# Performance work log

Hardware: AMD Instinct MI355X
Metric: run time of the kernel (lower is better)

## Reference

```python
import jax, jax.numpy as jnp
import numpy as np

LMAX = 3
NDEG = LMAX + 1            # degrees l = 0..3
MDIM = 2 * LMAX + 1        # padded m dimension (7)
K = 128                    # channels per degree
N = 4096                   # number of samples (atomic environments)
NITER = 2                  # number_of_iterations

# CG paths (l1, l2) -> L with |l1-l2| <= L <= min(l1+l2, LMAX); 34 paths
PATHS = [(l1, l2, L)
         for L in range(NDEG)
         for l1 in range(NDEG)
         for l2 in range(NDEG)
         if abs(l1 - l2) <= L <= l1 + l2]


def setup_inputs() -> dict:
    key = jax.random.key(0)
    k1, k2, k3, k4 = jax.random.split(key, 4)

    # zero-mask padded m components: valid m < 2l+1 per degree l
    mmask = (jnp.arange(MDIM)[None, :] < (2 * jnp.arange(NDEG) + 1)[:, None])
    mmask = mmask.astype(jnp.float32)                      # [NDEG, MDIM]

    feats = jax.random.normal(k1, (NDEG, N, MDIM, K), dtype=jnp.float32)
    feats = feats * mmask[:, None, :, None]

    # CG-like coefficients, zero-padded per path to [2l1+1, 2l2+1, 2L+1]
    umask = np.zeros((len(PATHS), MDIM, MDIM, MDIM), dtype=np.float32)
    for p, (l1, l2, L) in enumerate(PATHS):
        umask[p, :2 * l1 + 1, :2 * l2 + 1, :2 * L + 1] = 1.0
    U = jax.random.normal(k2, (len(PATHS), MDIM, MDIM, MDIM), dtype=jnp.float32)
    U = 0.1 * U * jnp.asarray(umask)

    scale = 1.0 / np.sqrt(K)
    mixer_W = scale * jax.random.normal(k3, (NITER + 1, NDEG, K, K), dtype=jnp.float32)
    iter_W = scale * jax.random.normal(k4, (NITER, NDEG, K, K), dtype=jnp.float32)

    return {"feats": feats, "U": U, "mixer_W": mixer_W, "iter_W": iter_W}


def spherical_linear(f, W):
    # per-degree channel mix: f [NDEG, N, MDIM, K], W [NDEG, K, K]
    return jnp.einsum('lnmk,lkj->lnmj', f, W)


def tensor_product(f1, f2, U):
    # channel-wise CG tensor product, summed over paths into each output degree L
    out = jnp.zeros_like(f1)
    for p, (l1, l2, L) in enumerate(PATHS):
        out = out.at[L].add(jnp.einsum('nak,nbk,abc->nck', f1[l1], f2[l2], U[p]))
    return out


def reference(feats, U, mixer_W, iter_W):
    # mixed_densities = [mixer(density) for mixer in self.mixers]
    mixed = [spherical_linear(feats, mixer_W[i]) for i in range(NITER + 1)]
    cur = mixed[0]
    # CG iterations: residual( linear( tensor_product(cur, mixed[t+1]) ) )
    for t in range(NITER):
        tp = tensor_product(cur, mixed[t + 1], U)
        cur = cur + spherical_linear(tp, iter_W[t])
    return cur
```

## Files before the change

kernel.cpp:

```cpp
#include <hip/hip_runtime.h>

#define NSAMP 4096
#define KCH   128
#define MDIM  7

typedef __attribute__((ext_vector_type(8))) short bf16x8;
typedef __attribute__((ext_vector_type(4))) float f32x4;
typedef __attribute__((ext_vector_type(4))) unsigned u32x4;

static constexpr int RB[4] = {0, 1, 4, 9};
static constexpr int RE[4] = {1, 4, 9, 16};
static constexpr int PR_L[16] = {0,1,1,1,2,2,2,2,2,3,3,3,3,3,3,3};
static constexpr int PR_M[16] = {0,0,1,2,0,1,2,3,4,0,1,2,3,4,5,6};

static constexpr int PIDX[4][4][4] = {
  { { 0,-1,-1,-1},{-1, 1,-1,-1},{-1,-1, 2,-1},{-1,-1,-1, 3} },
  { {-1, 4,-1,-1},{ 5, 6, 7,-1},{-1, 8, 9,10},{-1,-1,11,12} },
  { {-1,-1,13,-1},{-1,14,15,16},{17,18,19,20},{-1,21,22,23} },
  { {-1,-1,-1,24},{-1,-1,25,26},{-1,27,28,29},{30,31,32,33} }
};

static constexpr int ZL[12] = {0,0,0,0,0,0, 1,1,1,1, 2,2};
static constexpr int ZM[12] = {1,2,3,4,5,6, 3,4,5,6, 5,6};

#define WP_BYTES 1310720u
#define BG_BYTES 16384u

static __device__ __forceinline__ unsigned short f2bf(float x) {
    unsigned u = __builtin_bit_cast(unsigned, x);
    u = u + 0x7FFFu + ((u >> 16) & 1u);
    return (unsigned short)(u >> 16);
}
static __device__ __forceinline__ float bf2f(unsigned short h) {
    unsigned u = ((unsigned)h) << 16;
    return __builtin_bit_cast(float, u);
}

__global__ __launch_bounds__(256) void cg_prep(const float* __restrict__ mW,
                                               const float* __restrict__ iW,
                                               unsigned short* __restrict__ Wp)
{
    int gid = blockIdx.x * 256 + threadIdx.x;
    int lane = gid & 63;
    int set  = gid >> 6;
    int spl = set & 1;
    int ks  = (set >> 1) & 3;
    int ct  = (set >> 3) & 7;
    int l   = (set >> 6) & 3;
    int mi  = set >> 8;
    const float* src = (mi < 3) ? (mW + ((size_t)mi * 4 + l) * (KCH * KCH))
                                : (iW + ((size_t)(mi - 3) * 4 + l) * (KCH * KCH));
    int j  = ct * 16 + (lane & 15);
    int kb = ks * 32 + (lane >> 4) * 8;
    unsigned short o[8];
#pragma unroll
    for (int e = 0; e < 8; ++e) {
        float w = src[(size_t)(kb + e) * KCH + j];
        unsigned short h = f2bf(w);
        o[e] = spl ? f2bf(w - bf2f(h)) : h;
    }
    uint4 pk;
    unsigned* pw = (unsigned*)&pk;
#pragma unroll
    for (int q = 0; q < 4; ++q) pw[q] = (unsigned)o[2*q] | ((unsigned)o[2*q+1] << 16);
    *(uint4*)(Wp + (size_t)set * 512 + lane * 8) = pk;
}

__global__ __launch_bounds__(256) void cg_prepg(const float* __restrict__ U,
                                                unsigned short* __restrict__ Bg)
{
    const int gid  = blockIdx.x * 256 + threadIdx.x;
    const int s    = gid >> 7;
    const int spl  = (gid >> 6) & 1;
    const int lane = gid & 63;
    const int c    = lane & 15;
    const int kb   = s * 32 + (lane >> 4) * 8;
    const int Lo   = PR_L[c], cm = PR_M[c];
    unsigned short o[8];
#pragma unroll
    for (int e = 0; e < 8; ++e) {
        const int k  = kb + e;
        const int i  = k >> 4, j = k & 15;
        const int l1 = PR_L[i], a = PR_M[i];
        const int l2 = PR_L[j], b = PR_M[j];
        const int p  = PIDX[Lo][l1][l2];
        float val = (p >= 0) ? U[p * 343 + (a * 7 + b) * 7 + cm] : 0.0f;
        unsigned short h = f2bf(val);
        o[e] = spl ? f2bf(val - bf2f(h)) : h;
    }
    uint4 pk;
    unsigned* pw = (unsigned*)&pk;
#pragma unroll
    for (int q = 0; q < 4; ++q) pw[q] = (unsigned)o[2*q] | ((unsigned)o[2*q+1] << 16);
    *(uint4*)(Bg + (size_t)((s * 2 + spl) * 64 + lane) * 8) = pk;
}

static __device__ __forceinline__ bf16x8 ldF(const unsigned short* P, int row16, int key, int c) {
    int cs = c ^ (key & 7);
    return *(const bf16x8*)(P + row16 * 128 + cs * 8);
}

static __device__ __forceinline__ void stage_feats1(const float* __restrict__ feats,
                                                    unsigned short* Fh, int tid, int n0)
{
    const int row = tid >> 1;
    const int r   = row >> 4;
    const int nlr = row & 15;
    const int kh  = tid & 1;
    const int l = PR_L[r], m = PR_M[r];
    const float* g = feats + (((size_t)l * NSAMP + (n0 + nlr)) * MDIM + m) * KCH + kh * 64;
    unsigned short* fh = Fh + row * 128;
#pragma unroll
    for (int c8 = 0; c8 < 8; ++c8) {
        f32x4 a = *(const f32x4*)(g + c8 * 8);
        f32x4 b = *(const f32x4*)(g + c8 * 8 + 4);
        float v[8] = {a[0], a[1], a[2], a[3], b[0], b[1], b[2], b[3]};
        uint4 ph;
        unsigned* pw = (unsigned*)&ph;
#pragma unroll
        for (int q = 0; q < 4; ++q)
            pw[q] = (unsigned)f2bf(v[2*q]) | ((unsigned)f2bf(v[2*q+1]) << 16);
        const int cs = (kh * 8 + c8) ^ (nlr & 7);
        *(uint4*)(fh + cs * 8) = ph;
    }
}

static __device__ __forceinline__ void mix_sweep1(const unsigned short* Fh,
                                                  const bf16x8* __restrict__ Wp, int mi,
                                                  int ct, int lane, f32x4 (&acc)[16])
{
    const int kg = lane >> 4;
    const int l15 = lane & 15;
#pragma unroll
    for (int r = 0; r < 16; ++r) { acc[r][0]=acc[r][1]=acc[r][2]=acc[r][3]=0.0f; }
#pragma unroll
    for (int ks = 0; ks < 4; ++ks) {
#pragma unroll
        for (int l = 0; l < 4; ++l) {
            const int s0 = (((mi * 4 + l) * 8 + ct) * 4 + ks) * 2;
            bf16x8 bh = Wp[(size_t)s0 * 64 + lane];
            bf16x8 bl = Wp[(size_t)(s0 + 1) * 64 + lane];
#pragma unroll
            for (int r = RB[l]; r < RE[l]; ++r) {
                bf16x8 ah = ldF(Fh, r * 16 + l15, l15, ks * 4 + kg);
                acc[r] = __builtin_amdgcn_mfma_f32_16x16x32_bf16(ah, bh, acc[r], 0, 0, 0);
                acc[r] = __builtin_amdgcn_mfma_f32_16x16x32_bf16(ah, bl, acc[r], 0, 0, 0);
            }
        }
    }
}

static __device__ __forceinline__ void mix_sweep2(const unsigned short* Fh,
                                                  const bf16x8* __restrict__ Wp, int ma, int mb,
                                                  int ct, int lane,
                                                  f32x4 (&acc0)[16], f32x4 (&acc1)[16])
{
    const int kg = lane >> 4;
    const int l15 = lane & 15;
#pragma unroll
    for (int r = 0; r < 16; ++r) {
        acc0[r][0]=acc0[r][1]=acc0[r][2]=acc0[r][3]=0.0f;
        acc1[r][0]=acc1[r][1]=acc1[r][2]=acc1[r][3]=0.0f;
    }
#pragma unroll
    for (int ks = 0; ks < 4; ++ks) {
#pragma unroll
        for (int l = 0; l < 4; ++l) {
            const int s0 = (((ma * 4 + l) * 8 + ct) * 4 + ks) * 2;
            const int s1 = (((mb * 4 + l) * 8 + ct) * 4 + ks) * 2;
            bf16x8 b0h = Wp[(size_t)s0 * 64 + lane];
            bf16x8 b0l = Wp[(size_t)(s0 + 1) * 64 + lane];
            bf16x8 b1h = Wp[(size_t)s1 * 64 + lane];
            bf16x8 b1l = Wp[(size_t)(s1 + 1) * 64 + lane];
#pragma unroll
            for (int r = RB[l]; r < RE[l]; ++r) {
                bf16x8 ah = ldF(Fh, r * 16 + l15, l15, ks * 4 + kg);
                acc0[r] = __builtin_amdgcn_mfma_f32_16x16x32_bf16(ah, b0h, acc0[r], 0, 0, 0);
                acc0[r] = __builtin_amdgcn_mfma_f32_16x16x32_bf16(ah, b0l, acc0[r], 0, 0, 0);
                acc1[r] = __builtin_amdgcn_mfma_f32_16x16x32_bf16(ah, b1h, acc1[r], 0, 0, 0);
                acc1[r] = __builtin_amdgcn_mfma_f32_16x16x32_bf16(ah, b1l, acc1[r], 0, 0, 0);
            }
        }
    }
}

static __device__ __forceinline__ void acc_to_lds(const f32x4 (&acc)[16], unsigned short* P,
                                                  int ct, int lane)
{
    const int kg = lane >> 4;
    const int l15 = lane & 15;
    const int chnk = ct * 2 + (l15 >> 3);
#pragma unroll
    for (int r = 0; r < 16; ++r) {
#pragma unroll
        for (int q = 0; q < 4; ++q) {
            const int smp = kg * 4 + q;
            const int cs = chnk ^ (smp & 7);
            P[(smp * 16 + r) * 128 + cs * 8 + (l15 & 7)] = f2bf(acc[r][q]);
        }
    }
}

static __device__ __forceinline__ void tp_iter(unsigned short* Ch, const unsigned short* Mt,
                                               const bf16x8* __restrict__ Bg,
                                               const bf16x8* __restrict__ Wp, int miW,
                                               int ct, int lane, f32x4 (&racc)[16])
{
    const int kg  = lane >> 4;
    const int l15 = lane & 15;
    const int i0 = kg >> 1;
    const int j0 = (kg & 1) * 8;
    const int chnk = ct * 2 + (l15 >> 3);
    const int chA  = ct * 2 + (kg >> 1);
    const int co4  = (kg * 4) & 7;

    bf16x8 bgh[8], bgl[8];
#pragma unroll
    for (int s = 0; s < 8; ++s) {
        bgh[s] = Bg[(size_t)(s * 2 + 0) * 64 + lane];
        bgl[s] = Bg[(size_t)(s * 2 + 1) * 64 + lane];
    }

    f32x4 tpa[8];
#pragma unroll 1
    for (int g = 0; g < 2; ++g) {
#pragma unroll
        for (int uu = 0; uu < 8; ++uu) {
            const int u = g * 8 + uu;
            const int cs = chnk ^ (u & 7);
            const unsigned short* cb = Ch + u * 2048 + cs * 8 + (l15 & 7);
            const unsigned short* mb = Mt + u * 2048 + cs * 8 + (l15 & 7);
            float cvv[8], mvv[8];
#pragma unroll
            for (int s = 0; s < 8; ++s) cvv[s] = bf2f(cb[(i0 + 2 * s) * 128]);
#pragma unroll
            for (int e = 0; e < 8; ++e) mvv[e] = bf2f(mb[(j0 + e) * 128]);
            f32x4 acc = {0.0f, 0.0f, 0.0f, 0.0f};
#pragma unroll
            for (int s = 0; s < 8; ++s) {
                float pf[8];
#pragma unroll
                for (int e = 0; e < 8; ++e) pf[e] = cvv[s] * mvv[e];
                unsigned ah[4];
#pragma unroll
                for (int d = 0; d < 4; ++d) {
                    asm("v_cvt_pk_bf16_f32 %0, %1, %2" : "=v"(ah[d]) : "v"(pf[2*d]), "v"(pf[2*d+1]));
                }
                const u32x4 AH = {ah[0], ah[1], ah[2], ah[3]};
                const bf16x8 a_h = __builtin_bit_cast(bf16x8, AH);
                acc = __builtin_amdgcn_mfma_f32_16x16x32_bf16(a_h, bgh[s], acc, 0, 0, 0);
                acc = __builtin_amdgcn_mfma_f32_16x16x32_bf16(a_h, bgl[s], acc, 0, 0, 0);
            }
            tpa[uu] = acc;
        }
        __syncthreads();
#pragma unroll
        for (int uu = 0; uu < 8; ++uu) {
            const int u = g * 8 + uu;
            const int cs = chA ^ ((u ^ l15) & 7);
            const int soff = (u * 16 + l15) * 128 + cs * 8 + co4;
            const unsigned short h0 = f2bf(tpa[uu][0]);
            const unsigned short h1 = f2bf(tpa[uu][1]);
            const unsigned short h2 = f2bf(tpa[uu][2]);
            const unsigned short h3 = f2bf(tpa[uu][3]);
            *(unsigned*)(Ch + soff)     = (unsigned)h0 | ((unsigned)h1 << 16);
            *(unsigned*)(Ch + soff + 2) = (unsigned)h2 | ((unsigned)h3 << 16);
        }
    }
    __syncthreads();

#pragma unroll
    for (int ks = 0; ks < 4; ++ks) {
#pragma unroll
        for (int l = 0; l < 4; ++l) {
            const int s0 = (((miW * 4 + l) * 8 + ct) * 4 + ks) * 2;
            bf16x8 bh = Wp[(size_t)s0 * 64 + lane];
            bf16x8 bl = Wp[(size_t)(s0 + 1) * 64 + lane];
#pragma unroll
            for (int r = RB[l]; r < RE[l]; ++r) {
                bf16x8 ah = ldF(Ch, l15 * 16 + r, l15 ^ r, ks * 4 + kg);
                racc[r] = __builtin_amdgcn_mfma_f32_16x16x32_bf16(ah, bh, racc[r], 0, 0, 0);
                racc[r] = __builtin_amdgcn_mfma_f32_16x16x32_bf16(ah, bl, racc[r], 0, 0, 0);
            }
        }
    }
}

__global__ __launch_bounds__(512, 2) void cg_fuseA(const float* __restrict__ feats,
                                                   const bf16x8* __restrict__ Wp,
                                                   const bf16x8* __restrict__ Bg,
                                                   unsigned short* __restrict__ Pcur,
                                                   int base)
{
    extern __shared__ char smem[];
    unsigned short* Fh = (unsigned short*)smem;
    unsigned short* Tp = Fh + 32768;

    const int tid  = threadIdx.x;
    const int lane = tid & 63;
    const int ct   = tid >> 6;
    const int nl0  = blockIdx.x * 16;
    const int kg   = lane >> 4;
    const int l15  = lane & 15;
    const int j    = ct * 16 + l15;

    stage_feats1(feats, Fh, tid, base + nl0);
    __syncthreads();

    f32x4 accC[16], accM[16];
    mix_sweep2(Fh, Wp, 0, 1, ct, lane, accC, accM);
    __syncthreads();

    acc_to_lds(accC, Fh, ct, lane);
    acc_to_lds(accM, Tp, ct, lane);
    __syncthreads();
    tp_iter(Fh, Tp, Bg, Wp, 3, ct, lane, accC);

#pragma unroll
    for (int r = 0; r < 16; ++r) {
#pragma unroll
        for (int q = 0; q < 4; ++q) {
            const int nl = nl0 + kg * 4 + q;
            Pcur[((size_t)nl * 16 + r) * KCH + j] = f2bf(accC[r][q]);
        }
    }
}

__global__ __launch_bounds__(512, 2) void cg_fuseB(const float* __restrict__ feats,
                                                   const bf16x8* __restrict__ Wp,
                                                   const bf16x8* __restrict__ Bg,
                                                   const unsigned short* __restrict__ Pcur,
                                                   float* __restrict__ gout,
                                                   int base)
{
    extern __shared__ char smem[];
    unsigned short* Fh = (unsigned short*)smem;
    unsigned short* Tp = Fh + 32768;

    const int tid  = threadIdx.x;
    const int lane = tid & 63;
    const int ct   = tid >> 6;
    const int nl0  = blockIdx.x * 16;
    const int kg   = lane >> 4;
    const int l15  = lane & 15;
    const int j    = ct * 16 + l15;

    f32x4 racc[16];
#pragma unroll
    for (int r = 0; r < 16; ++r) {
#pragma unroll
        for (int q = 0; q < 4; ++q) {
            const int nl = nl0 + kg * 4 + q;
            racc[r][q] = bf2f(Pcur[((size_t)nl * 16 + r) * KCH + j]);
        }
    }

    stage_feats1(feats, Fh, tid, base + nl0);
    __syncthreads();

    f32x4 accM[16];
    mix_sweep1(Fh, Wp, 2, ct, lane, accM);
    __syncthreads();

    acc_to_lds(racc, Fh, ct, lane);
    acc_to_lds(accM, Tp, ct, lane);
    __syncthreads();
    tp_iter(Fh, Tp, Bg, Wp, 4, ct, lane, racc);

#pragma unroll
    for (int r = 0; r < 16; ++r) {
#pragma unroll
        for (int q = 0; q < 4; ++q) {
            const int n = base + nl0 + kg * 4 + q;
            gout[(((size_t)PR_L[r] * NSAMP + n) * MDIM + PR_M[r]) * KCH + j] = racc[r][q];
        }
    }
    {
        const int j2 = tid & 127;
        const int g  = tid >> 7;
#pragma unroll
        for (int z = 0; z < 12; ++z) {
#pragma unroll
            for (int i = 0; i < 4; ++i) {
                const int n = base + nl0 + g * 4 + i;
                gout[(((size_t)ZL[z] * NSAMP + n) * MDIM + ZM[z]) * KCH + j2] = 0.0f;
            }
        }
    }
}

extern "C" void kernel_launch(void* const* d_in, const int* in_sizes, int n_in,
                              void* d_out, int out_size, void* d_ws, size_t ws_size,
                              hipStream_t stream)
{
    const float* feats = (const float*)d_in[0];
    const float* U     = (const float*)d_in[1];
    const float* mW    = (const float*)d_in[2];
    const float* iW    = (const float*)d_in[3];
    float* out = (float*)d_out;

    const size_t fixed = (size_t)WP_BYTES + BG_BYTES;
    size_t avail = (ws_size > fixed) ? (ws_size - fixed) : 0;
    int NC = (int)(avail / 4096);
    NC = (NC / 16) * 16;
    if (NC > NSAMP) NC = NSAMP;
    if (NC < 16) return;

    char* wsb = (char*)d_ws;
    unsigned short* Wp   = (unsigned short*)wsb;
    unsigned short* Bg   = (unsigned short*)(wsb + WP_BYTES);
    unsigned short* Pcur = (unsigned short*)(wsb + fixed);

    hipFuncSetAttribute(reinterpret_cast<const void*>(cg_fuseA),
                        hipFuncAttributeMaxDynamicSharedMemorySize, 131072);
    hipFuncSetAttribute(reinterpret_cast<const void*>(cg_fuseB),
                        hipFuncAttributeMaxDynamicSharedMemorySize, 131072);

    cg_prep<<<320, 256, 0, stream>>>(mW, iW, Wp);
    cg_prepg<<<4, 256, 0, stream>>>(U, Bg);

    for (int base = 0; base < NSAMP; base += NC) {
        const int nc = (NSAMP - base < NC) ? (NSAMP - base) : NC;
        cg_fuseA<<<nc / 16, 512, 131072, stream>>>(feats, (const bf16x8*)Wp,
                                                   (const bf16x8*)Bg, Pcur, base);
        cg_fuseB<<<nc / 16, 512, 131072, stream>>>(feats, (const bf16x8*)Wp,
                                                   (const bf16x8*)Bg, Pcur, out, base);
    }
}
```

Before: 95.91 us.

## Transpose tensor-product LDS staging to vectorized per-channel layout

Changes the LDS staging of the current and mixed features from a sample-major, per-element bf16 layout to a channel-major XOR-swizzled layout. Writes become packed 16-byte stores and tensor-product reads become three 16-byte loads per u instead of sixteen scalar loads. The two-group TP loop with a mid-loop barrier is replaced by a single pass over all 16 u that keeps 16 accumulators live before writing back. This cuts LDS instruction count and barriers at the cost of higher register pressure under the 512-thread, 2-block launch bounds.

```diff
diff --git a/kernel.cpp b/kernel.cpp
--- a/kernel.cpp
+++ b/kernel.cpp
@@ -34,6 +34,12 @@
 static __device__ __forceinline__ float bf2f(unsigned short h) {
     unsigned u = ((unsigned)h) << 16;
     return __builtin_bit_cast(float, u);
+}
+static __device__ __forceinline__ float lo2f(unsigned w) {
+    return __builtin_bit_cast(float, w << 16);
+}
+static __device__ __forceinline__ float hi2f(unsigned w) {
+    return __builtin_bit_cast(float, w & 0xFFFF0000u);
 }
 
 __global__ __launch_bounds__(256) void cg_prep(const float* __restrict__ mW,
@@ -184,91 +190,110 @@
     }
 }
 
-static __device__ __forceinline__ void acc_to_lds(const f32x4 (&acc)[16], unsigned short* P,
-                                                  int ct, int lane)
+static __device__ __forceinline__ void acc_to_ldsT(const f32x4 (&acc)[16], unsigned short* T,
+                                                   int ct, int lane)
 {
     const int kg = lane >> 4;
     const int l15 = lane & 15;
-    const int chnk = ct * 2 + (l15 >> 3);
-#pragma unroll
-    for (int r = 0; r < 16; ++r) {
-#pragma unroll
-        for (int q = 0; q < 4; ++q) {
-            const int smp = kg * 4 + q;
-            const int cs = chnk ^ (smp & 7);
-            P[(smp * 16 + r) * 128 + cs * 8 + (l15 & 7)] = f2bf(acc[r][q]);
-        }
-    }
-}
-
-static __device__ __forceinline__ void tp_iter(unsigned short* Ch, const unsigned short* Mt,
-                                               const bf16x8* __restrict__ Bg,
-                                               const bf16x8* __restrict__ Wp, int miW,
-                                               int ct, int lane, f32x4 (&racc)[16])
+    unsigned short* tb = T + (ct * 16 + l15) * 256;
+    const int key = l15 & 7;
+#pragma unroll
+    for (int q = 0; q < 4; ++q) {
+        const int smp = kg * 4 + q;
+#pragma unroll
+        for (int half = 0; half < 2; ++half) {
+            const int c = smp * 2 + half;
+            const int p = (c & 24) | ((c & 7) ^ key);
+            u32x4 pk;
+#pragma unroll
+            for (int d = 0; d < 4; ++d) {
+                unsigned w;
+                asm("v_cvt_pk_bf16_f32 %0, %1, %2"
+                    : "=v"(w) : "v"(acc[half * 8 + 2 * d][q]), "v"(acc[half * 8 + 2 * d + 1][q]));
+                pk[d] = w;
+            }
+            *(u32x4*)(tb + p * 8) = pk;
+        }
+    }
+}
+
+static __device__ __forceinline__ void tp_computeT(const unsigned short* CurT,
+                                                   const unsigned short* MtT,
+                                                   const bf16x8 (&bgh)[8], const bf16x8 (&bgl)[8],
+                                                   int ct, int lane, f32x4 (&tpa)[16])
 {
     const int kg  = lane >> 4;
     const int l15 = lane & 15;
     const int i0 = kg >> 1;
-    const int j0 = (kg & 1) * 8;
-    const int chnk = ct * 2 + (l15 >> 3);
-    const int chA  = ct * 2 + (kg >> 1);
-    const int co4  = (kg * 4) & 7;
-
-    bf16x8 bgh[8], bgl[8];
-#pragma unroll
-    for (int s = 0; s < 8; ++s) {
-        bgh[s] = Bg[(size_t)(s * 2 + 0) * 64 + lane];
-        bgl[s] = Bg[(size_t)(s * 2 + 1) * 64 + lane];
-    }
-
-    f32x4 tpa[8];
-#pragma unroll 1
-    for (int g = 0; g < 2; ++g) {
-#pragma unroll
-        for (int uu = 0; uu < 8; ++uu) {
-            const int u = g * 8 + uu;
-            const int cs = chnk ^ (u & 7);
-            const unsigned short* cb = Ch + u * 2048 + cs * 8 + (l15 & 7);
-            const unsigned short* mb = Mt + u * 2048 + cs * 8 + (l15 & 7);
-            float cvv[8], mvv[8];
-#pragma unroll
-            for (int s = 0; s < 8; ++s) cvv[s] = bf2f(cb[(i0 + 2 * s) * 128]);
-#pragma unroll
-            for (int e = 0; e < 8; ++e) mvv[e] = bf2f(mb[(j0 + e) * 128]);
-            f32x4 acc = {0.0f, 0.0f, 0.0f, 0.0f};
-#pragma unroll
-            for (int s = 0; s < 8; ++s) {
-                float pf[8];
-#pragma unroll
-                for (int e = 0; e < 8; ++e) pf[e] = cvv[s] * mvv[e];
-                unsigned ah[4];
-#pragma unroll
-                for (int d = 0; d < 4; ++d) {
-                    asm("v_cvt_pk_bf16_f32 %0, %1, %2" : "=v"(ah[d]) : "v"(pf[2*d]), "v"(pf[2*d+1]));
-                }
-                const u32x4 AH = {ah[0], ah[1], ah[2], ah[3]};
-                const bf16x8 a_h = __builtin_bit_cast(bf16x8, AH);
-                acc = __builtin_amdgcn_mfma_f32_16x16x32_bf16(a_h, bgh[s], acc, 0, 0, 0);
-                acc = __builtin_amdgcn_mfma_f32_16x16x32_bf16(a_h, bgl[s], acc, 0, 0, 0);
-            }
-            tpa[uu] = acc;
-        }
-        __syncthreads();
-#pragma unroll
-        for (int uu = 0; uu < 8; ++uu) {
-            const int u = g * 8 + uu;
-            const int cs = chA ^ ((u ^ l15) & 7);
-            const int soff = (u * 16 + l15) * 128 + cs * 8 + co4;
-            const unsigned short h0 = f2bf(tpa[uu][0]);
-            const unsigned short h1 = f2bf(tpa[uu][1]);
-            const unsigned short h2 = f2bf(tpa[uu][2]);
-            const unsigned short h3 = f2bf(tpa[uu][3]);
-            *(unsigned*)(Ch + soff)     = (unsigned)h0 | ((unsigned)h1 << 16);
-            *(unsigned*)(Ch + soff + 2) = (unsigned)h2 | ((unsigned)h3 << 16);
-        }
-    }
-    __syncthreads();
-
+    const int j0h = (kg & 1);
+    const unsigned short* cb = CurT + (ct * 16 + l15) * 256;
+    const unsigned short* mb = MtT  + (ct * 16 + l15) * 256;
+    const int key = l15 & 7;
+#pragma unroll
+    for (int u = 0; u < 16; ++u) {
+        const int c0 = u * 2, c1 = u * 2 + 1, cm = u * 2 + j0h;
+        const int p0 = (c0 & 24) | ((c0 & 7) ^ key);
+        const int p1 = (c1 & 24) | ((c1 & 7) ^ key);
+        const int pm = (cm & 24) | ((cm & 7) ^ key);
+        const u32x4 A0 = *(const u32x4*)(cb + p0 * 8);
+        const u32x4 A1 = *(const u32x4*)(cb + p1 * 8);
+        const u32x4 M0 = *(const u32x4*)(mb + pm * 8);
+        float cvv[8], mvv[8];
+#pragma unroll
+        for (int s = 0; s < 4; ++s) {
+            cvv[s]     = i0 ? hi2f(A0[s]) : lo2f(A0[s]);
+            cvv[4 + s] = i0 ? hi2f(A1[s]) : lo2f(A1[s]);
+        }
+#pragma unroll
+        for (int e = 0; e < 8; ++e) {
+            mvv[e] = (e & 1) ? hi2f(M0[e >> 1]) : lo2f(M0[e >> 1]);
+        }
+        f32x4 acc = {0.0f, 0.0f, 0.0f, 0.0f};
+#pragma unroll
+        for (int s = 0; s < 8; ++s) {
+            float pf[8];
+#pragma unroll
+            for (int e = 0; e < 8; ++e) pf[e] = cvv[s] * mvv[e];
+            unsigned ah[4];
+#pragma unroll
+            for (int d = 0; d < 4; ++d) {
+                asm("v_cvt_pk_bf16_f32 %0, %1, %2" : "=v"(ah[d]) : "v"(pf[2*d]), "v"(pf[2*d+1]));
+            }
+            const u32x4 AH = {ah[0], ah[1], ah[2], ah[3]};
+            const bf16x8 a_h = __builtin_bit_cast(bf16x8, AH);
+            acc = __builtin_amdgcn_mfma_f32_16x16x32_bf16(a_h, bgh[s], acc, 0, 0, 0);
+            acc = __builtin_amdgcn_mfma_f32_16x16x32_bf16(a_h, bgl[s], acc, 0, 0, 0);
+        }
+        tpa[u] = acc;
+    }
+}
+
+static __device__ __forceinline__ void tp_writeAll(unsigned short* P, int ct, int lane,
+                                                   const f32x4 (&tpa)[16])
+{
+    const int kg  = lane >> 4;
+    const int l15 = lane & 15;
+    const int chA = ct * 2 + (kg >> 1);
+    const int co4 = (kg * 4) & 7;
+#pragma unroll
+    for (int u = 0; u < 16; ++u) {
+        const int cs = chA ^ ((u ^ l15) & 7);
+        const int soff = (u * 16 + l15) * 128 + cs * 8 + co4;
+        const unsigned short h0 = f2bf(tpa[u][0]);
+        const unsigned short h1 = f2bf(tpa[u][1]);
+        const unsigned short h2 = f2bf(tpa[u][2]);
+        const unsigned short h3 = f2bf(tpa[u][3]);
+        *(unsigned*)(P + soff)     = (unsigned)h0 | ((unsigned)h1 << 16);
+        *(unsigned*)(P + soff + 2) = (unsigned)h2 | ((unsigned)h3 << 16);
+    }
+}
+
+static __device__ __forceinline__ void iter_sweep(const unsigned short* Tp,
+                                                  const bf16x8* __restrict__ Wp, int miW,
+                                                  int ct, int lane, f32x4 (&racc)[16])
+{
+    const int kg = lane >> 4;
+    const int l15 = lane & 15;
 #pragma unroll
     for (int ks = 0; ks < 4; ++ks) {
 #pragma unroll
@@ -278,12 +303,31 @@
             bf16x8 bl = Wp[(size_t)(s0 + 1) * 64 + lane];
 #pragma unroll
             for (int r = RB[l]; r < RE[l]; ++r) {
-                bf16x8 ah = ldF(Ch, l15 * 16 + r, l15 ^ r, ks * 4 + kg);
+                bf16x8 ah = ldF(Tp, l15 * 16 + r, l15 ^ r, ks * 4 + kg);
                 racc[r] = __builtin_amdgcn_mfma_f32_16x16x32_bf16(ah, bh, racc[r], 0, 0, 0);
                 racc[r] = __builtin_amdgcn_mfma_f32_16x16x32_bf16(ah, bl, racc[r], 0, 0, 0);
             }
         }
     }
+}
+
+static __device__ __forceinline__ void tp_iterT(unsigned short* CurT, const unsigned short* MtT,
+                                                const bf16x8* __restrict__ Bg,
+                                                const bf16x8* __restrict__ Wp, int miW,
+                                                int ct, int lane, f32x4 (&racc)[16])
+{
+    bf16x8 bgh[8], bgl[8];
+#pragma unroll
+    for (int s = 0; s < 8; ++s) {
+        bgh[s] = Bg[(size_t)(s * 2 + 0) * 64 + lane];
+        bgl[s] = Bg[(size_t)(s * 2 + 1) * 64 + lane];
+    }
+    f32x4 tpa[16];
+    tp_computeT(CurT, MtT, bgh, bgl, ct, lane, tpa);
+    __syncthreads();
+    tp_writeAll(CurT, ct, lane, tpa);
+    __syncthreads();
+    iter_sweep(CurT, Wp, miW, ct, lane, racc);
 }
 
 __global__ __launch_bounds__(512, 2) void cg_fuseA(const float* __restrict__ feats,
@@ -311,10 +355,10 @@
     mix_sweep2(Fh, Wp, 0, 1, ct, lane, accC, accM);
     __syncthreads();
 
-    acc_to_lds(accC, Fh, ct, lane);
-    acc_to_lds(accM, Tp, ct, lane);
-    __syncthreads();
-    tp_iter(Fh, Tp, Bg, Wp, 3, ct, lane, accC);
+    acc_to_ldsT(accC, Fh, ct, lane);
+    acc_to_ldsT(accM, Tp, ct, lane);
+    __syncthreads();
+    tp_iterT(Fh, Tp, Bg, Wp, 3, ct, lane, accC);
 
 #pragma unroll
     for (int r = 0; r < 16; ++r) {
@@ -362,10 +406,10 @@
     mix_sweep1(Fh, Wp, 2, ct, lane, accM);
     __syncthreads();
 
-    acc_to_lds(racc, Fh, ct, lane);
-    acc_to_lds(accM, Tp, ct, lane);
-    __syncthreads();
-    tp_iter(Fh, Tp, Bg, Wp, 4, ct, lane, racc);
+    acc_to_ldsT(racc, Fh, ct, lane);
+    acc_to_ldsT(accM, Tp, ct, lane);
+    __syncthreads();
+    tp_iterT(Fh, Tp, Bg, Wp, 4, ct, lane, racc);
 
 #pragma unroll
     for (int r = 0; r < 16; ++r) {
```

Result: slower. 98.85 us (+3.1%).
